# Optimization experiments

Measured on AMD Instinct MI355X. Metric: run time of the kernel, lower is better.

The kernel has to match this reference:

```python
import jax, jax.numpy as jnp
import numpy as np

DIM = 256
HEADS = 8
HEAD_DIM = DIM // HEADS
WS = 8
EPS = 1e-5


def layernorm(x, g, b):
    mu = jnp.mean(x, axis=-1, keepdims=True)
    var = jnp.var(x, axis=-1, keepdims=True)
    return (x - mu) * jax.lax.rsqrt(var + EPS) * g + b


def partition_windows(x, ws):
    B, H, W, C = x.shape
    x = x.reshape(B, H // ws, ws, W // ws, ws, C)
    x = jnp.transpose(x, (0, 1, 3, 2, 4, 5))
    return x.reshape(B * (H // ws) * (W // ws), ws * ws, C)


def unpartition_windows(x, ws, B, H, W):
    C = x.shape[-1]
    x = x.reshape(B, H // ws, W // ws, ws, ws, C)
    x = jnp.transpose(x, (0, 1, 3, 2, 4, 5))
    return x.reshape(B, H, W, C)


def setup_inputs() -> dict:
    key = jax.random.key(0)
    ks = jax.random.split(key, 14)
    B, H, W, C = 16, 64, 64, DIM
    s_in = 1.0 / np.sqrt(C)
    s_hid = 1.0 / np.sqrt(4 * C)
    return {
        "x": jax.random.normal(ks[0], (B, H, W, C), jnp.float32),
        "ln1_g": jnp.ones((C,), jnp.float32),
        "ln1_b": jnp.zeros((C,), jnp.float32),
        "qkv_w": jax.random.uniform(ks[1], (3 * C, C), jnp.float32, -s_in, s_in),
        "qkv_b": jax.random.uniform(ks[2], (3 * C,), jnp.float32, -s_in, s_in),
        "proj_w": jax.random.uniform(ks[3], (C, C), jnp.float32, -s_in, s_in),
        "proj_b": jax.random.uniform(ks[4], (C,), jnp.float32, -s_in, s_in),
        "ln2_g": jnp.ones((C,), jnp.float32),
        "ln2_b": jnp.zeros((C,), jnp.float32),
        "ffn_w1": jax.random.uniform(ks[5], (4 * C, C), jnp.float32, -s_in, s_in),
        "ffn_b1": jax.random.uniform(ks[6], (4 * C,), jnp.float32, -s_in, s_in),
        "ffn_w2": jax.random.uniform(ks[7], (C, 4 * C), jnp.float32, -s_hid, s_hid),
        "ffn_b2": jax.random.uniform(ks[8], (C,), jnp.float32, -s_hid, s_hid),
    }


def attention(blocks, qkv_w, qkv_b, proj_w, proj_b):
    # blocks: [Bn, N, C]
    Bn, N, C = blocks.shape
    qkv = blocks @ qkv_w.T + qkv_b  # [Bn, N, 3C]
    qkv = qkv.reshape(Bn, N, 3, HEADS, HEAD_DIM)
    q, k, v = qkv[:, :, 0], qkv[:, :, 1], qkv[:, :, 2]  # each [Bn, N, h, d]
    # Faithful to the source: q @ k^T over the last two dims -> head-x-head scores per token
    scores = jnp.einsum("bnhd,bngd->bnhg", q, k) / np.sqrt(HEAD_DIM)
    attn = jax.nn.softmax(scores, axis=-1)
    out = jnp.einsum("bnhg,bngd->bnhd", attn, v).reshape(Bn, N, C)
    return out @ proj_w.T + proj_b


def reference(x, ln1_g, ln1_b, qkv_w, qkv_b, proj_w, proj_b,
              ln2_g, ln2_b, ffn_w1, ffn_b1, ffn_w2, ffn_b2):
    B, H, W, C = x.shape
    x_ = layernorm(x, ln1_g, ln1_b)
    blocks = partition_windows(x_, WS)  # [B*nW, ws*ws, C]
    out = attention(blocks, qkv_w, qkv_b, proj_w, proj_b)
    x = x + unpartition_windows(out, WS, B, H, W)
    x_ = layernorm(x, ln2_g, ln2_b)
    x_ = jax.nn.relu(x_ @ ffn_w1.T + ffn_b1) @ ffn_w2.T + ffn_b2
    return x + x_
```

## Files before the change

kernel.cpp:

```cpp
#include <hip/hip_runtime.h>
#include <hip/hip_bf16.h>
#include <stdint.h>

typedef float f32x4 __attribute__((ext_vector_type(4)));
typedef __bf16 bf16x8 __attribute__((ext_vector_type(8)));
typedef unsigned short ushort8 __attribute__((ext_vector_type(8)));

__device__ __forceinline__ float bf2f(unsigned short u) {
    unsigned int x = ((unsigned int)u) << 16;
    return __builtin_bit_cast(float, x);
}
__device__ __forceinline__ unsigned short f2bf(float f) {
    unsigned int x = __builtin_bit_cast(unsigned int, f);
    unsigned int lsb = (x >> 16) & 1u;
    x += 0x7fffu + lsb;
    return (unsigned short)(x >> 16);
}

#define GLL16(gptr, lptr)                                                      \
    __builtin_amdgcn_global_load_lds(                                          \
        (const __attribute__((address_space(1))) void*)(gptr),                 \
        (__attribute__((address_space(3))) void*)(lptr), 16, 0, 0)

#define VMWAIT(N)                                                              \
    do { asm volatile("s_waitcnt vmcnt(" #N ")" ::: "memory"); } while (0)
#define BARRIER_NODRAIN()                                                      \
    do {                                                                       \
        asm volatile("s_waitcnt lgkmcnt(0)" ::: "memory");                     \
        __builtin_amdgcn_s_barrier();                                          \
    } while (0)

__global__ __launch_bounds__(256) void cvt4_kernel(
    const float* __restrict__ w0, const float* __restrict__ w1,
    const float* __restrict__ w2, const float* __restrict__ w3,
    unsigned short* __restrict__ dst)
{
    const int i = blockIdx.x * 256 + threadIdx.x;
    const float* s; int off;
    if      (i <  49152) { s = w0; off = 0; }
    else if (i <  65536) { s = w1; off = 49152; }
    else if (i < 131072) { s = w2; off = 65536; }
    else                 { s = w3; off = 131072; }
    f32x4 v = ((const f32x4*)s)[i - off];
    ushort4 o;
    o.x = f2bf(v.x); o.y = f2bf(v.y); o.z = f2bf(v.z); o.w = f2bf(v.w);
    ((ushort4*)dst)[i] = o;
}

__global__ __launch_bounds__(256) void ln_kernel(
    const float* __restrict__ x, const float* __restrict__ g,
    const float* __restrict__ b, unsigned short* __restrict__ y)
{
    const int lane = threadIdx.x & 63, wave = threadIdx.x >> 6;
    const size_t tok = (size_t)blockIdx.x * 4 + wave;
    f32x4 v = *(const f32x4*)(x + tok * 256 + lane * 4);
    float s = v.x + v.y + v.z + v.w;
    float q = v.x * v.x + v.y * v.y + v.z * v.z + v.w * v.w;
#pragma unroll
    for (int o = 32; o; o >>= 1) {
        s += __shfl_xor(s, o, 64);
        q += __shfl_xor(q, o, 64);
    }
    float mean = s * (1.f / 256.f);
    float var  = q * (1.f / 256.f) - mean * mean;
    float rstd = rsqrtf(var + 1e-5f);
    f32x4 gr = *(const f32x4*)(g + lane * 4);
    f32x4 br = *(const f32x4*)(b + lane * 4);
    ushort4 o4;
    o4.x = f2bf((v.x - mean) * rstd * gr.x + br.x);
    o4.y = f2bf((v.y - mean) * rstd * gr.y + br.y);
    o4.z = f2bf((v.z - mean) * rstd * gr.z + br.z);
    o4.w = f2bf((v.w - mean) * rstd * gr.w + br.w);
    *(ushort4*)(y + tok * 256 + lane * 4) = o4;
}

template <int RELU, int HASRES, int OUTF32>
__global__ __launch_bounds__(256) void gemm_bt(
    const unsigned short* __restrict__ A,
    const unsigned short* __restrict__ W,
    const float* __restrict__ bias,
    const float* res,
    void* Cv,
    int M, int N, int K, int nby)
{
    __shared__ __align__(16) unsigned short As[128 * 64];
    __shared__ __align__(16) unsigned short Bs[128 * 64];

    const int t    = threadIdx.x;
    const int id   = blockIdx.x;
    const int xcd  = id & 7;
    const int sl   = id >> 3;
    const int by   = sl % nby;
    const int bx   = (sl / nby) * 8 + xcd;
    const int m0   = bx * 128;
    const int n0   = by * 128;
    const int lane = t & 63;
    const int wave = t >> 6;
    const int wm = wave & 1, wn = wave >> 1;
    const int lr = lane & 15, kc = lane >> 4;

    f32x4 acc[4][4] = {};

    const int rA   = t >> 3;
    const int gcol = ((t & 7) ^ (rA & 7)) * 8;
    const unsigned short* gA = A + (size_t)(m0 + rA) * K + gcol;
    const unsigned short* gB = W + (size_t)(n0 + rA) * K + gcol;

    for (int k0 = 0; k0 < K; k0 += 64) {
#pragma unroll
        for (int w = 0; w < 4; ++w) {
            GLL16(gA + (size_t)(w * 32) * K + k0, &As[(w * 256 + t) * 8]);
            GLL16(gB + (size_t)(w * 32) * K + k0, &Bs[(w * 256 + t) * 8]);
        }
        __syncthreads();

#pragma unroll
        for (int hh = 0; hh < 2; ++hh) {
            bf16x8 af[4], bf[4];
#pragma unroll
            for (int i = 0; i < 4; ++i) {
                const int ra = wm * 64 + i * 16 + lr;
                const int rb = wn * 64 + i * 16 + lr;
                af[i] = *(const bf16x8*)&As[ra * 64 + ((hh * 4 + kc) ^ (ra & 7)) * 8];
                bf[i] = *(const bf16x8*)&Bs[rb * 64 + ((hh * 4 + kc) ^ (rb & 7)) * 8];
            }
#pragma unroll
            for (int i = 0; i < 4; ++i)
#pragma unroll
                for (int j = 0; j < 4; ++j)
                    acc[i][j] = __builtin_amdgcn_mfma_f32_16x16x32_bf16(
                        af[i], bf[j], acc[i][j], 0, 0, 0);
        }
        __syncthreads();
    }

    float* Cf = (float*)Cv;
    unsigned short* Cb = (unsigned short*)Cv;
    const int row0 = m0 + wm * 64;
    const int col0 = n0 + wn * 64;
    const int cl = lane & 15;
    const int rq = (lane >> 4) * 4;
#pragma unroll
    for (int i = 0; i < 4; ++i) {
#pragma unroll
        for (int j = 0; j < 4; ++j) {
            const int col = col0 + j * 16 + cl;
            const float bv = bias[col];
#pragma unroll
            for (int r = 0; r < 4; ++r) {
                const int row = row0 + i * 16 + rq + r;
                float v = acc[i][j][r] + bv;
                if (RELU) v = fmaxf(v, 0.f);
                const size_t o = (size_t)row * N + col;
                if (HASRES) v += res[o];
                if (OUTF32) Cf[o] = v;
                else        Cb[o] = f2bf(v);
            }
        }
    }
}

__global__ __launch_bounds__(256) void attn_headmix(
    const unsigned short* __restrict__ qkv,
    unsigned short* __restrict__ out,
    int T)
{
    const int lane = threadIdx.x & 63, wave = threadIdx.x >> 6;
    const int tok = blockIdx.x * 4 + wave;
    if (tok >= T) return;
    const unsigned short* base = qkv + (size_t)tok * 768;
    const int h = lane >> 3, g = lane & 7;

    float s = 0.f;
#pragma unroll
    for (int d8 = 0; d8 < 4; ++d8) {
        ushort4 qa = *(const ushort4*)(base + h * 32 + d8 * 8);
        ushort4 qb = *(const ushort4*)(base + h * 32 + d8 * 8 + 4);
        ushort4 ka = *(const ushort4*)(base + 256 + g * 32 + d8 * 8);
        ushort4 kb = *(const ushort4*)(base + 256 + g * 32 + d8 * 8 + 4);
        s += bf2f(qa.x) * bf2f(ka.x) + bf2f(qa.y) * bf2f(ka.y)
           + bf2f(qa.z) * bf2f(ka.z) + bf2f(qa.w) * bf2f(ka.w)
           + bf2f(qb.x) * bf2f(kb.x) + bf2f(qb.y) * bf2f(kb.y)
           + bf2f(qb.z) * bf2f(kb.z) + bf2f(qb.w) * bf2f(kb.w);
    }
    s *= 0.17677669529663687f;

    float mx = s;
#pragma unroll
    for (int o = 1; o < 8; o <<= 1) mx = fmaxf(mx, __shfl_xor(mx, o, 64));
    float e = __expf(s - mx);
    float sum = e;
#pragma unroll
    for (int o = 1; o < 8; o <<= 1) sum += __shfl_xor(sum, o, 64);
    const float a = e / sum;

    float o0 = 0.f, o1 = 0.f, o2 = 0.f, o3 = 0.f;
#pragma unroll
    for (int gg = 0; gg < 8; ++gg) {
        const float ag = __shfl(a, (lane & 56) | gg, 64);
        ushort4 vv = *(const ushort4*)(base + 512 + gg * 32 + g * 4);
        o0 += ag * bf2f(vv.x);
        o1 += ag * bf2f(vv.y);
        o2 += ag * bf2f(vv.z);
        o3 += ag * bf2f(vv.w);
    }
    ushort4 ov;
    ov.x = f2bf(o0); ov.y = f2bf(o1); ov.z = f2bf(o2); ov.w = f2bf(o3);
    *(ushort4*)(out + (size_t)tok * 256 + lane * 4) = ov;
}

__global__ __launch_bounds__(512, 2) void ffn_fused(
    float* xo,
    const float* __restrict__ ln2_g, const float* __restrict__ ln2_b,
    const unsigned short* __restrict__ w1,
    const float* __restrict__ b1p,
    const unsigned short* __restrict__ w2,
    const float* __restrict__ b2p)
{
    __shared__ __align__(16) unsigned short U[32768];
    __shared__ __align__(16) unsigned short W1a[16384];
    __shared__ __align__(16) unsigned short W2a[16384];
    __shared__ __align__(16) unsigned short Hs[2][8192];

    unsigned short* const W1b = U;
    unsigned short* const W2b = U + 16384;

    const int t = threadIdx.x;
    const int lane = t & 63, wave = t >> 6;
    const int m0 = blockIdx.x * 128;
    const int lr = lane & 15, kc = lane >> 4;
    const int cl = lane & 15, rq = (lane >> 4) * 4;
    const int wm = wave & 1, wn = wave >> 1;

    const int r1b = t >> 5;
    const int sc1 = t & 31;
    const int gc1 = (sc1 & ~7) | ((sc1 & 7) ^ (r1b & 7));
    const int r2b = t >> 3;
    const int gc2 = (t & 7) ^ (r2b & 7);

    #define STAGE_W1(hp, W1t)                                                  \
        do {                                                                   \
            _Pragma("unroll")                                                  \
            for (int j = 0; j < 4; ++j)                                        \
                GLL16(w1 + (size_t)((hp) * 64 + j * 16 + r1b) * 256 + gc1 * 8, \
                      &(W1t)[(j * 512 + t) * 8]);                              \
        } while (0)
    #define STAGE_W2(hp, W2t)                                                  \
        do {                                                                   \
            _Pragma("unroll")                                                  \
            for (int j = 0; j < 4; ++j)                                        \
                GLL16(w2 + (size_t)(j * 64 + r2b) * 1024 + (hp) * 64 + gc2 * 8,\
                      &(W2t)[(j * 512 + t) * 8]);                              \
        } while (0)

    STAGE_W1(0, W1a);
    STAGE_W2(0, W2a);
    f32x4 bvc = *(const f32x4*)(b1p + wn * 16 + rq);

    {
        const int row0 = t >> 2;
        const int seg  = t & 3;
        const float* xrp = xo + (size_t)(m0 + row0) * 256 + seg * 64;
        f32x4 xv[16];
#pragma unroll
        for (int i = 0; i < 16; ++i) xv[i] = ((const f32x4*)xrp)[i];
        float s = 0.f, q = 0.f;
#pragma unroll
        for (int i = 0; i < 16; ++i) {
            s += xv[i].x + xv[i].y + xv[i].z + xv[i].w;
            q += xv[i].x * xv[i].x + xv[i].y * xv[i].y
               + xv[i].z * xv[i].z + xv[i].w * xv[i].w;
        }
        s += __shfl_xor(s, 1, 64); q += __shfl_xor(q, 1, 64);
        s += __shfl_xor(s, 2, 64); q += __shfl_xor(q, 2, 64);
        const float mean = s * (1.f / 256.f);
        const float rstd = rsqrtf(q * (1.f / 256.f) - mean * mean + 1e-5f);
#pragma unroll
        for (int c8 = 0; c8 < 8; ++c8) {
            const f32x4 g0 = ((const f32x4*)(ln2_g + seg * 64 + c8 * 8))[0];
            const f32x4 g1 = ((const f32x4*)(ln2_g + seg * 64 + c8 * 8))[1];
            const f32x4 bb0 = ((const f32x4*)(ln2_b + seg * 64 + c8 * 8))[0];
            const f32x4 bb1 = ((const f32x4*)(ln2_b + seg * 64 + c8 * 8))[1];
            const f32x4 a0 = xv[c8 * 2], a1 = xv[c8 * 2 + 1];
            ushort8 o;
            o[0] = f2bf((a0.x - mean) * rstd * g0.x + bb0.x);
            o[1] = f2bf((a0.y - mean) * rstd * g0.y + bb0.y);
            o[2] = f2bf((a0.z - mean) * rstd * g0.z + bb0.z);
            o[3] = f2bf((a0.w - mean) * rstd * g0.w + bb0.w);
            o[4] = f2bf((a1.x - mean) * rstd * g1.x + bb1.x);
            o[5] = f2bf((a1.y - mean) * rstd * g1.y + bb1.y);
            o[6] = f2bf((a1.z - mean) * rstd * g1.z + bb1.z);
            o[7] = f2bf((a1.w - mean) * rstd * g1.w + bb1.w);
            const int gc = seg * 8 + c8;
            const int sc = (gc & ~7) | ((gc & 7) ^ (row0 & 7));
            *(ushort8*)&U[row0 * 256 + sc * 8] = o;
        }
    }
    __syncthreads();

    bf16x8 afr[4][8];
#pragma unroll
    for (int i = 0; i < 4; ++i) {
        const int ra = wm * 64 + i * 16 + lr;
#pragma unroll
        for (int ks = 0; ks < 8; ++ks) {
            const int c = ks * 4 + kc;
            afr[i][ks] = *(const bf16x8*)
                &U[ra * 256 + ((c & ~7) | ((c & 7) ^ (ra & 7))) * 8];
        }
    }
    __syncthreads();

    f32x4 acc[4][4] = {};

    #define HPHASE(bv, W1c, Hbuf)                                              \
        do {                                                                   \
            f32x4 acch[4] = {};                                                \
            __builtin_amdgcn_s_setprio(1);                                     \
            _Pragma("unroll")                                                  \
            for (int ks = 0; ks < 8; ++ks) {                                   \
                const int c = ks * 4 + kc;                                     \
                const int rb = wn * 16 + lr;                                   \
                const bf16x8 bfr = *(const bf16x8*)                            \
                    &(W1c)[rb * 256 + ((c & ~7) | ((c & 7) ^ (rb & 7))) * 8];  \
                _Pragma("unroll")                                              \
                for (int i = 0; i < 4; ++i)                                    \
                    acch[i] = __builtin_amdgcn_mfma_f32_16x16x32_bf16(         \
                        bfr, afr[i][ks], acch[i], 0, 0, 0);                    \
            }                                                                  \
            __builtin_amdgcn_s_setprio(0);                                     \
            const int sbase = wn * 2 + (rq >> 3);                              \
            _Pragma("unroll")                                                  \
            for (int i = 0; i < 4; ++i) {                                      \
                const int tok = wm * 64 + i * 16 + cl;                         \
                ushort4 o;                                                     \
                o.x = f2bf(fmaxf(acch[i][0] + (bv).x, 0.f));                   \
                o.y = f2bf(fmaxf(acch[i][1] + (bv).y, 0.f));                   \
                o.z = f2bf(fmaxf(acch[i][2] + (bv).z, 0.f));                   \
                o.w = f2bf(fmaxf(acch[i][3] + (bv).w, 0.f));                   \
                *(ushort4*)&(Hbuf)[tok * 64 + ((sbase ^ (tok & 7)) * 8)        \
                                   + (rq & 4)] = o;                            \
            }                                                                  \
        } while (0)

    #define OPHASE(W2c, Hbuf)                                                  \
        do {                                                                   \
            _Pragma("unroll")                                                  \
            for (int ks = 0; ks < 2; ++ks) {                                   \
                const int c = ks * 4 + kc;                                     \
                bf16x8 bw[4];                                                  \
                _Pragma("unroll")                                              \
                for (int j = 0; j < 4; ++j) {                                  \
                    const int rb = wn * 64 + j * 16 + lr;                      \
                    bw[j] = *(const bf16x8*)                                   \
                        &(W2c)[rb * 64 + ((c ^ (rb & 7)) * 8)];                \
                }                                                              \
                __builtin_amdgcn_s_setprio(1);                                 \
                _Pragma("unroll")                                              \
                for (int i = 0; i < 4; ++i) {                                  \
                    const int ra = wm * 64 + i * 16 + lr;                      \
                    const bf16x8 ah = *(const bf16x8*)                         \
                        &(Hbuf)[ra * 64 + ((c ^ (ra & 7)) * 8)];               \
                    _Pragma("unroll")                                          \
                    for (int j = 0; j < 4; ++j)                                \
                        acc[i][j] = __builtin_amdgcn_mfma_f32_16x16x32_bf16(   \
                            ah, bw[j], acc[i][j], 0, 0, 0);                    \
                }                                                              \
                __builtin_amdgcn_s_setprio(0);                                 \
            }                                                                  \
        } while (0)

    STAGE_W1(1, W1b);
    f32x4 bvn = *(const f32x4*)(b1p + 1 * 64 + wn * 16 + rq);
    HPHASE(bvc, W1a, Hs[0]);
    BARRIER_NODRAIN();
    bvc = bvn;

    STAGE_W1(2, W1a);
    STAGE_W2(1, W2b);
    bvn = *(const f32x4*)(b1p + 2 * 64 + wn * 16 + rq);
    VMWAIT(9);
    HPHASE(bvc, W1b, Hs[1]);
    OPHASE(W2a, Hs[0]);
    BARRIER_NODRAIN();
    bvc = bvn;

    for (int hc = 1; hc <= 13; ++hc) {
        unsigned short* const w1dst = (hc & 1) ? W1b : W1a;
        unsigned short* const w2dst = (hc & 1) ? W2a : W2b;
        unsigned short* const w1src = (hc & 1) ? W1a : W1b;
        unsigned short* const w2src = (hc & 1) ? W2b : W2a;
        STAGE_W1(hc + 2, w1dst);
        STAGE_W2(hc + 1, w2dst);
        bvn = *(const f32x4*)(b1p + (hc + 2) * 64 + wn * 16 + rq);
        VMWAIT(9);
        HPHASE(bvc, w1src, Hs[(hc + 1) & 1]);
        OPHASE(w2src, Hs[hc & 1]);
        BARRIER_NODRAIN();
        bvc = bvn;
    }

    STAGE_W2(15, W2b);
    VMWAIT(4);
    HPHASE(bvc, W1b, Hs[1]);
    OPHASE(W2a, Hs[0]);
    BARRIER_NODRAIN();

    VMWAIT(0);
    OPHASE(W2b, Hs[1]);

    const int rqe = (lane >> 4) * 4;
#pragma unroll
    for (int i = 0; i < 4; ++i)
#pragma unroll
        for (int j = 0; j < 4; ++j) {
            const int col = wn * 64 + j * 16 + cl;
            const float bv = b2p[col];
#pragma unroll
            for (int r = 0; r < 4; ++r) {
                const int row = m0 + wm * 64 + i * 16 + rqe + r;
                const size_t o = (size_t)row * 256 + col;
                xo[o] = acc[i][j][r] + bv + xo[o];
            }
        }
    #undef STAGE_W1
    #undef STAGE_W2
    #undef HPHASE
    #undef OPHASE
}

extern "C" void kernel_launch(void* const* d_in, const int* in_sizes, int n_in,
                              void* d_out, int out_size, void* d_ws, size_t ws_size,
                              hipStream_t stream)
{
    const float* x      = (const float*)d_in[0];
    const float* ln1_g  = (const float*)d_in[1];
    const float* ln1_b  = (const float*)d_in[2];
    const float* qkv_w  = (const float*)d_in[3];
    const float* qkv_b  = (const float*)d_in[4];
    const float* proj_w = (const float*)d_in[5];
    const float* proj_b = (const float*)d_in[6];
    const float* ln2_g  = (const float*)d_in[7];
    const float* ln2_b  = (const float*)d_in[8];
    const float* ffn_w1 = (const float*)d_in[9];
    const float* ffn_b1 = (const float*)d_in[10];
    const float* ffn_w2 = (const float*)d_in[11];
    const float* ffn_b2 = (const float*)d_in[12];
    float* xo = (float*)d_out;

    const int M = 65536;
    const size_t MEG = 1024 * 1024;
    unsigned short* ws = (unsigned short*)d_ws;
    unsigned short* qkv_wb  = ws;
    unsigned short* proj_wb = ws + 196608;
    unsigned short* ffn_w1b = ws + 262144;
    unsigned short* ffn_w2b = ws + 524288;
    unsigned short* xn   = ws + 1 * MEG;
    unsigned short* att  = ws + 17 * MEG;
    unsigned short* qkvb = ws + 33 * MEG;

    cvt4_kernel<<<768, 256, 0, stream>>>(qkv_w, proj_w, ffn_w1, ffn_w2, ws);

    ln_kernel<<<M / 4, 256, 0, stream>>>(x, ln1_g, ln1_b, xn);
    gemm_bt<0, 0, 0><<<3072, 256, 0, stream>>>(
        xn, qkv_wb, qkv_b, nullptr, qkvb, M, 768, 256, 6);
    attn_headmix<<<M / 4, 256, 0, stream>>>(qkvb, att, M);
    gemm_bt<0, 1, 1><<<1024, 256, 0, stream>>>(
        att, proj_wb, proj_b, x, xo, M, 256, 256, 2);
    ffn_fused<<<M / 128, 512, 0, stream>>>(
        xo, ln2_g, ln2_b, ffn_w1b, ffn_b1, ffn_w2b, ffn_b2);
}
```

Measured before the change: 406.9 us.

## Restructure FFN inner loop into barrier-separated load/MFMA phases

Splits the fused FFN hidden and output phases into smaller phases. Each phase loads its LDS fragments up front, then a workgroup barrier and a single lgkmcnt wait gate a dense MFMA burst, with another barrier after it. The W2 staging and vmcnt waits are reordered to fit the new phases. The aim is to keep waves in lockstep so LDS reads and MFMA execution alternate cleanly across waves. In exchange it adds many more barriers per iteration, which can cause stalls.

Measured after the change: 412.7 us. About the same (+1.4%).

```diff
diff --git a/kernel.cpp b/kernel.cpp
--- a/kernel.cpp
+++ b/kernel.cpp
@@ -24,11 +24,6 @@
 
 #define VMWAIT(N)                                                              \
     do { asm volatile("s_waitcnt vmcnt(" #N ")" ::: "memory"); } while (0)
-#define BARRIER_NODRAIN()                                                      \
-    do {                                                                       \
-        asm volatile("s_waitcnt lgkmcnt(0)" ::: "memory");                     \
-        __builtin_amdgcn_s_barrier();                                          \
-    } while (0)
 
 __global__ __launch_bounds__(256) void cvt4_kernel(
     const float* __restrict__ w0, const float* __restrict__ w1,
@@ -256,6 +251,7 @@
     STAGE_W1(0, W1a);
     STAGE_W2(0, W2a);
     f32x4 bvc = *(const f32x4*)(b1p + wn * 16 + rq);
+    f32x4 bvn;
 
     {
         const int row0 = t >> 2;
@@ -313,22 +309,62 @@
 
     f32x4 acc[4][4] = {};
 
-    #define HPHASE(bv, W1c, Hbuf)                                              \
+    #define PHASE_H(W1c, ksb)                                                  \
         do {                                                                   \
-            f32x4 acch[4] = {};                                                \
+            bf16x8 bfr_[4];                                                    \
+            _Pragma("unroll")                                                  \
+            for (int kk = 0; kk < 4; ++kk) {                                   \
+                const int c = ((ksb) + kk) * 4 + kc;                           \
+                const int rb = wn * 16 + lr;                                   \
+                bfr_[kk] = *(const bf16x8*)                                    \
+                    &(W1c)[rb * 256 + ((c & ~7) | ((c & 7) ^ (rb & 7))) * 8];  \
+            }                                                                  \
+            __builtin_amdgcn_s_barrier();                                      \
+            asm volatile("s_waitcnt lgkmcnt(0)" ::: "memory");                 \
+            __builtin_amdgcn_sched_barrier(0);                                 \
             __builtin_amdgcn_s_setprio(1);                                     \
             _Pragma("unroll")                                                  \
-            for (int ks = 0; ks < 8; ++ks) {                                   \
-                const int c = ks * 4 + kc;                                     \
-                const int rb = wn * 16 + lr;                                   \
-                const bf16x8 bfr = *(const bf16x8*)                            \
-                    &(W1c)[rb * 256 + ((c & ~7) | ((c & 7) ^ (rb & 7))) * 8];  \
+            for (int kk = 0; kk < 4; ++kk)                                     \
                 _Pragma("unroll")                                              \
                 for (int i = 0; i < 4; ++i)                                    \
                     acch[i] = __builtin_amdgcn_mfma_f32_16x16x32_bf16(         \
-                        bfr, afr[i][ks], acch[i], 0, 0, 0);                    \
+                        bfr_[kk], afr[i][(ksb) + kk], acch[i], 0, 0, 0);       \
+            __builtin_amdgcn_s_setprio(0);                                     \
+            __builtin_amdgcn_s_barrier();                                      \
+        } while (0)
+
+    #define PHASE_O(W2c, Hbuf, ksel)                                           \
+        do {                                                                   \
+            const int c = (ksel) * 4 + kc;                                     \
+            bf16x8 bw_[4], ah_[4];                                             \
+            _Pragma("unroll")                                                  \
+            for (int j = 0; j < 4; ++j) {                                      \
+                const int rb = wn * 64 + j * 16 + lr;                          \
+                bw_[j] = *(const bf16x8*)                                      \
+                    &(W2c)[rb * 64 + ((c ^ (rb & 7)) * 8)];                    \
             }                                                                  \
+            _Pragma("unroll")                                                  \
+            for (int i = 0; i < 4; ++i) {                                      \
+                const int ra = wm * 64 + i * 16 + lr;                          \
+                ah_[i] = *(const bf16x8*)                                      \
+                    &(Hbuf)[ra * 64 + ((c ^ (ra & 7)) * 8)];                   \
+            }                                                                  \
+            __builtin_amdgcn_s_barrier();                                      \
+            asm volatile("s_waitcnt lgkmcnt(0)" ::: "memory");                 \
+            __builtin_amdgcn_sched_barrier(0);                                 \
+            __builtin_amdgcn_s_setprio(1);                                     \
+            _Pragma("unroll")                                                  \
+            for (int i = 0; i < 4; ++i)                                        \
+                _Pragma("unroll")                                              \
+                for (int j = 0; j < 4; ++j)                                    \
+                    acc[i][j] = __builtin_amdgcn_mfma_f32_16x16x32_bf16(       \
+                        ah_[i], bw_[j], acc[i][j], 0, 0, 0);                   \
             __builtin_amdgcn_s_setprio(0);                                     \
+            __builtin_amdgcn_s_barrier();                                      \
+        } while (0)
+
+    #define HSTORE(bv, Hbuf)                                                   \
+        do {                                                                   \
             const int sbase = wn * 2 + (rq >> 3);                              \
             _Pragma("unroll")                                                  \
             for (int i = 0; i < 4; ++i) {                                      \
@@ -343,46 +379,29 @@
             }                                                                  \
         } while (0)
 
-    #define OPHASE(W2c, Hbuf)                                                  \
-        do {                                                                   \
-            _Pragma("unroll")                                                  \
-            for (int ks = 0; ks < 2; ++ks) {                                   \
-                const int c = ks * 4 + kc;                                     \
-                bf16x8 bw[4];                                                  \
-                _Pragma("unroll")                                              \
-                for (int j = 0; j < 4; ++j) {                                  \
-                    const int rb = wn * 64 + j * 16 + lr;                      \
-                    bw[j] = *(const bf16x8*)                                   \
-                        &(W2c)[rb * 64 + ((c ^ (rb & 7)) * 8)];                \
-                }                                                              \
-                __builtin_amdgcn_s_setprio(1);                                 \
-                _Pragma("unroll")                                              \
-                for (int i = 0; i < 4; ++i) {                                  \
-                    const int ra = wm * 64 + i * 16 + lr;                      \
-                    const bf16x8 ah = *(const bf16x8*)                         \
-                        &(Hbuf)[ra * 64 + ((c ^ (ra & 7)) * 8)];               \
-                    _Pragma("unroll")                                          \
-                    for (int j = 0; j < 4; ++j)                                \
-                        acc[i][j] = __builtin_amdgcn_mfma_f32_16x16x32_bf16(   \
-                            ah, bw[j], acc[i][j], 0, 0, 0);                    \
-                }                                                              \
-                __builtin_amdgcn_s_setprio(0);                                 \
-            }                                                                  \
-        } while (0)
-
     STAGE_W1(1, W1b);
-    f32x4 bvn = *(const f32x4*)(b1p + 1 * 64 + wn * 16 + rq);
-    HPHASE(bvc, W1a, Hs[0]);
-    BARRIER_NODRAIN();
+    {
+        f32x4 acch[4] = {};
+        PHASE_H(W1a, 0);
+        bvn = *(const f32x4*)(b1p + 1 * 64 + wn * 16 + rq);
+        PHASE_H(W1a, 4);
+        HSTORE(bvc, Hs[0]);
+    }
     bvc = bvn;
 
     STAGE_W1(2, W1a);
+    VMWAIT(5);
+    {
+        f32x4 acch[4] = {};
+        PHASE_H(W1b, 0);
+        bvn = *(const f32x4*)(b1p + 2 * 64 + wn * 16 + rq);
+        PHASE_H(W1b, 4);
+        HSTORE(bvc, Hs[1]);
+    }
     STAGE_W2(1, W2b);
-    bvn = *(const f32x4*)(b1p + 2 * 64 + wn * 16 + rq);
     VMWAIT(9);
-    HPHASE(bvc, W1b, Hs[1]);
-    OPHASE(W2a, Hs[0]);
-    BARRIER_NODRAIN();
+    PHASE_O(W2a, Hs[0], 0);
+    PHASE_O(W2a, Hs[0], 1);
     bvc = bvn;
 
     for (int hc = 1; hc <= 13; ++hc) {
@@ -390,24 +409,39 @@
         unsigned short* const w2dst = (hc & 1) ? W2a : W2b;
         unsigned short* const w1src = (hc & 1) ? W1a : W1b;
         unsigned short* const w2src = (hc & 1) ? W2b : W2a;
+        unsigned short* const hdst = Hs[(hc + 1) & 1];
+        unsigned short* const hsrc = Hs[hc & 1];
         STAGE_W1(hc + 2, w1dst);
+        VMWAIT(9);
+        {
+            f32x4 acch[4] = {};
+            PHASE_H(w1src, 0);
+            bvn = *(const f32x4*)(b1p + (hc + 2) * 64 + wn * 16 + rq);
+            PHASE_H(w1src, 4);
+            HSTORE(bvc, hdst);
+        }
         STAGE_W2(hc + 1, w2dst);
-        bvn = *(const f32x4*)(b1p + (hc + 2) * 64 + wn * 16 + rq);
         VMWAIT(9);
-        HPHASE(bvc, w1src, Hs[(hc + 1) & 1]);
-        OPHASE(w2src, Hs[hc & 1]);
-        BARRIER_NODRAIN();
+        PHASE_O(w2src, hsrc, 0);
+        PHASE_O(w2src, hsrc, 1);
         bvc = bvn;
     }
 
+    VMWAIT(5);
+    {
+        f32x4 acch[4] = {};
+        PHASE_H(W1b, 0);
+        PHASE_H(W1b, 4);
+        HSTORE(bvc, Hs[1]);
+    }
     STAGE_W2(15, W2b);
     VMWAIT(4);
-    HPHASE(bvc, W1b, Hs[1]);
-    OPHASE(W2a, Hs[0]);
-    BARRIER_NODRAIN();
+    PHASE_O(W2a, Hs[0], 0);
+    PHASE_O(W2a, Hs[0], 1);
 
     VMWAIT(0);
-    OPHASE(W2b, Hs[1]);
+    PHASE_O(W2b, Hs[1], 0);
+    PHASE_O(W2b, Hs[1], 1);
 
     const int rqe = (lane >> 4) * 4;
 #pragma unroll
@@ -425,8 +459,9 @@
         }
     #undef STAGE_W1
     #undef STAGE_W2
-    #undef HPHASE
-    #undef OPHASE
+    #undef PHASE_H
+    #undef PHASE_O
+    #undef HSTORE
 }
 
 extern "C" void kernel_launch(void* const* d_in, const int* in_sizes, int n_in,
```
